# Kernel tuning notes

Hardware: AMD Instinct MI355X
Metric: run time of the kernel (lower is better)

Reference implementation:

```python
import jax, jax.numpy as jnp
import numpy as np

BLOCK = 64      # block_size
NRAND = 3       # num_random_blocks
NUM_HEAD = 16
HEAD_DIM = 64
HIDDEN = 1024
PEN = -10000.0  # HF attn_mask_penalty


def _sparse_attn(q, k, v, band_mask, from_mask, to_mask, blocked_mask, rand_attn):
    # q,k,v: [B,H,S,D]; BigBird block-sparse attention (HF math).
    B, H, S, D = q.shape
    b, r = BLOCK, NRAND
    n = S // b
    rsd = 1.0 / (D ** 0.5)

    bq = q.reshape(B, H, n, b, D)
    bk = k.reshape(B, H, n, b, D)
    bv = v.reshape(B, H, n, b, D)

    bi = jnp.arange(B)[:, None, None, None]
    hi = jnp.arange(H)[None, :, None, None]
    # gathered random key/value blocks: [B,H,n-2,r*b,D]
    gk = bk[bi, hi, rand_attn].reshape(B, H, n - 2, r * b, D)
    gv = bv[bi, hi, rand_attn].reshape(B, H, n - 2, r * b, D)
    # random-block mask: [B,H,n-2,b,r*b]
    rm = blocked_mask[bi, rand_attn].reshape(B, H, n - 2, r * b)
    rand_mask = jnp.einsum("blq,bhlk->bhlqk", blocked_mask[:, 1:-1], rm)

    ones = lambda shp: jnp.ones(shp, q.dtype)

    # ---- first query block: attends to everything ----
    p = jnp.einsum("bhqd,bhkd->bhqk", bq[:, :, 0], k) * rsd + (1.0 - to_mask) * PEN
    c0 = jnp.einsum("bhqk,bhkd->bhqd", jax.nn.softmax(p, -1), v)[:, :, None]

    # ---- second query block: blocks 0,1,2,last + random ----
    k1 = jnp.concatenate([bk[:, :, 0], bk[:, :, 1], bk[:, :, 2], bk[:, :, -1], gk[:, :, 0]], axis=2)
    v1 = jnp.concatenate([bv[:, :, 0], bv[:, :, 1], bv[:, :, 2], bv[:, :, -1], gv[:, :, 0]], axis=2)
    p = jnp.einsum("bhqd,bhkd->bhqk", bq[:, :, 1], k1) * rsd
    seq_pad = jnp.concatenate([to_mask[..., :3 * b], to_mask[..., -b:], ones((B, 1, 1, r * b))], axis=3)
    rand_pad = jnp.concatenate([ones((B, H, b, 4 * b)), rand_mask[:, :, 0]], axis=3)
    p = p + (1.0 - jnp.minimum(seq_pad, rand_pad)) * PEN
    c1 = jnp.einsum("bhqk,bhkd->bhqd", jax.nn.softmax(p, -1), v1)[:, :, None]

    # ---- middle blocks 2..n-3: band(3 blocks) + first + last + random ----
    ek = jnp.concatenate([bk[:, :, 1:-3], bk[:, :, 2:-2], bk[:, :, 3:-1]], axis=3)  # [B,H,n-4,3b,D]
    ev = jnp.concatenate([bv[:, :, 1:-3], bv[:, :, 2:-2], bv[:, :, 3:-1]], axis=3)
    mq = bq[:, :, 2:-2]                                                              # [B,H,n-4,b,D]
    inner = jnp.einsum("bhlqd,bhlkd->bhlqk", mq, ek) * rsd + (1.0 - band_mask) * PEN
    randp = jnp.einsum("bhlqd,bhlkd->bhlqk", mq, gk[:, :, 1:-1]) * rsd + (1.0 - rand_mask[:, :, 1:-1]) * PEN
    firstp = jnp.einsum("bhlqd,bhkd->bhlqk", mq, bk[:, :, 0]) * rsd + (1.0 - to_mask[..., :b][:, :, None]) * PEN
    lastp = jnp.einsum("bhlqd,bhkd->bhlqk", mq, bk[:, :, -1]) * rsd + (1.0 - to_mask[..., -b:][:, :, None]) * PEN
    band = jnp.concatenate([firstp, inner, randp, lastp], axis=-1)  # [B,H,n-4,b,(5+r)*b]
    a = jax.nn.softmax(band, -1)
    cm = jnp.einsum("bhlqk,bhlkd->bhlqd", a[..., b:4 * b], ev)
    cm = cm + jnp.einsum("bhlqk,bhlkd->bhlqd", a[..., 4 * b:-b], gv[:, :, 1:-1])
    cm = cm + jnp.einsum("bhlqk,bhkd->bhlqd", a[..., :b], bv[:, :, 0])
    cm = cm + jnp.einsum("bhlqk,bhkd->bhlqd", a[..., -b:], bv[:, :, -1])

    # ---- second-last query block: blocks 0,-3,-2,-1 + random ----
    k2 = jnp.concatenate([bk[:, :, 0], bk[:, :, -3], bk[:, :, -2], bk[:, :, -1], gk[:, :, -1]], axis=2)
    v2 = jnp.concatenate([bv[:, :, 0], bv[:, :, -3], bv[:, :, -2], bv[:, :, -1], gv[:, :, -1]], axis=2)
    p = jnp.einsum("bhqd,bhkd->bhqk", bq[:, :, -2], k2) * rsd
    seq_pad = jnp.concatenate([to_mask[..., :b], to_mask[..., -3 * b:], ones((B, 1, 1, r * b))], axis=3)
    rand_pad = jnp.concatenate([ones((B, H, b, 4 * b)), rand_mask[:, :, -1]], axis=3)
    p = p + (1.0 - jnp.minimum(seq_pad, rand_pad)) * PEN
    c2 = jnp.einsum("bhqk,bhkd->bhqd", jax.nn.softmax(p, -1), v2)[:, :, None]

    # ---- last query block: attends to everything ----
    p = jnp.einsum("bhqd,bhkd->bhqk", bq[:, :, -1], k) * rsd + (1.0 - to_mask) * PEN
    c3 = jnp.einsum("bhqk,bhkd->bhqd", jax.nn.softmax(p, -1), v)[:, :, None]

    ctx = jnp.concatenate([c0, c1, cm, c2, c3], axis=2).reshape(B, H, S, D)
    ctx = ctx * from_mask  # [B,1,S,1]
    return ctx.transpose(0, 2, 1, 3).reshape(B, S, H * D)


def setup_inputs() -> dict:
    key = jax.random.key(0)
    ks = jax.random.split(key, 12)
    B, L = 2, 4064
    S = 4096
    n = S // BLOCK
    sc = 0.02
    inp = {
        "X": jax.random.normal(ks[0], (B, L, HIDDEN), jnp.float32),
        "Wq": jax.random.normal(ks[1], (HIDDEN, NUM_HEAD * HEAD_DIM), jnp.float32) * sc,
        "b_q": jnp.zeros((NUM_HEAD * HEAD_DIM,), jnp.float32),
        "Wk": jax.random.normal(ks[2], (HIDDEN, NUM_HEAD * HEAD_DIM), jnp.float32) * sc,
        "b_k": jnp.zeros((NUM_HEAD * HEAD_DIM,), jnp.float32),
        "Wv": jax.random.normal(ks[3], (HIDDEN, NUM_HEAD * HEAD_DIM), jnp.float32) * sc,
        "b_v": jnp.zeros((NUM_HEAD * HEAD_DIM,), jnp.float32),
        "Wo": jax.random.normal(ks[4], (NUM_HEAD * HEAD_DIM, HIDDEN), jnp.float32) * sc,
        "b_o": jnp.zeros((HIDDEN,), jnp.float32),
        "band_mask": jnp.ones((B, 1, n - 4, BLOCK, 3 * BLOCK), jnp.float32),
        "from_mask": jnp.ones((B, 1, S, 1), jnp.float32),
        "to_mask": jnp.ones((B, 1, 1, S), jnp.float32),
        "blocked_encoder_mask": jnp.ones((B, n, BLOCK), jnp.float32),
        "rand_attn": jax.random.randint(ks[5], (B, NUM_HEAD, n - 2, NRAND), 0, n, jnp.int32),
    }
    return inp


def reference(X, Wq, b_q, Wk, b_k, Wv, b_v, Wo, b_o,
              band_mask, from_mask, to_mask, blocked_encoder_mask, rand_attn):
    B, L, _ = X.shape
    pad = BLOCK - L % BLOCK  # matches torch wrapper (pads full block if L % b == 0)
    Xp = jnp.pad(X, ((0, 0), (0, pad), (0, 0)))
    S = L + pad

    def proj(W, bias):
        return (Xp @ W + bias).reshape(B, S, NUM_HEAD, HEAD_DIM).transpose(0, 2, 1, 3)

    q, k, v = proj(Wq, b_q), proj(Wk, b_k), proj(Wv, b_v)
    attn = _sparse_attn(q, k, v, band_mask, from_mask, to_mask, blocked_encoder_mask, rand_attn)
    out = attn @ Wo + b_o
    return out[:, :L]
```

## Files before the change

### kernel.cpp

```cpp
#include <hip/hip_runtime.h>

#define BB 2
#define SEQ 4096
#define LQ 4064
#define HID 1024
#define NH 16
#define HD 64
#define NB 64
#define BLK 64
#define NR 3
#define PENV -10000.0f

typedef __bf16 bf16;
typedef __bf16 bf16x8 __attribute__((ext_vector_type(8)));
typedef float floatx4 __attribute__((ext_vector_type(4)));

__device__ inline floatx4 mfma16(bf16x8 a, bf16x8 b, floatx4 c) {
    return __builtin_amdgcn_mfma_f32_16x16x32_bf16(a, b, c, 0, 0, 0);
}

__device__ inline void async_ld16(const bf16* g, bf16* l) {
    __builtin_amdgcn_global_load_lds(
        (const __attribute__((address_space(1))) unsigned int*)g,
        (__attribute__((address_space(3))) unsigned int*)l, 16, 0, 0);
}

__global__ __launch_bounds__(256) void cast_pad_x(const float* __restrict__ X,
                                                  bf16* __restrict__ Xp) {
    int t = blockIdx.x * 256 + threadIdx.x;
    int c4 = t & 255;
    int row = t >> 8;
    int b = row >> 12;
    int s = row & 4095;
    float4 v = make_float4(0.f, 0.f, 0.f, 0.f);
    if (s < LQ) {
        v = reinterpret_cast<const float4*>(X + ((size_t)(b * LQ + s)) * HID)[c4];
    }
    union { bf16 h[4]; uint2 u; } o;
    o.h[0] = (bf16)v.x; o.h[1] = (bf16)v.y; o.h[2] = (bf16)v.z; o.h[3] = (bf16)v.w;
    *reinterpret_cast<uint2*>(Xp + (size_t)row * HID + c4 * 4) = o.u;
}

__global__ __launch_bounds__(256) void transpose_w(const float* __restrict__ Wq,
                                                   const float* __restrict__ Wk,
                                                   const float* __restrict__ Wv,
                                                   const float* __restrict__ Wo,
                                                   bf16* __restrict__ WqkvT,
                                                   bf16* __restrict__ WoT) {
    __shared__ float tile[64][65];
    int sel = blockIdx.z;
    const float* src = (sel == 0) ? Wq : (sel == 1) ? Wk : (sel == 2) ? Wv : Wo;
    bf16* dst = (sel < 3) ? (WqkvT + (size_t)sel * HID * HID) : WoT;
    int j0 = blockIdx.x * 64, k0 = blockIdx.y * 64;
    int tx = threadIdx.x, ty = threadIdx.y;
    for (int i = 0; i < 16; i++) {
        int k = ty + i * 4;
        tile[k][tx] = src[(size_t)(k0 + k) * HID + j0 + tx];
    }
    __syncthreads();
    for (int i = 0; i < 16; i++) {
        int j = ty + i * 4;
        dst[(size_t)(j0 + j) * HID + k0 + tx] = (bf16)tile[tx][j];
    }
}

__global__ __launch_bounds__(256) void transpose_band(const float* __restrict__ band,
                                                      float* __restrict__ bandT) {
    __shared__ float tile[64][65];
    int kt = blockIdx.x;
    int lrow = blockIdx.y;
    int b = blockIdx.z;
    const float* src = band + ((size_t)(b * (NB - 4) + lrow) * BLK) * 192;
    float* dst = bandT + ((size_t)(b * (NB - 4) + lrow) * 192) * BLK;
    int tx = threadIdx.x, ty = threadIdx.y;
    for (int i = 0; i < 16; i++) {
        int qq = i * 4 + ty;
        tile[qq][tx] = src[(size_t)qq * 192 + kt * 64 + tx];
    }
    __syncthreads();
    for (int i = 0; i < 16; i++) {
        int k = i * 4 + ty;
        dst[(size_t)(kt * 64 + k) * BLK + tx] = tile[tx][k];
    }
}

__global__ __launch_bounds__(256) void gemm_qkv(const bf16* __restrict__ Xp,
                                                const bf16* __restrict__ WT,
                                                const float* __restrict__ bq,
                                                const float* __restrict__ bk,
                                                const float* __restrict__ bv,
                                                bf16* __restrict__ qo,
                                                bf16* __restrict__ ko,
                                                bf16* __restrict__ vt) {
    __shared__ __align__(16) char smem[36864];
    bf16* As = (bf16*)smem;
    bf16* Bs = As + 128 * 64;
    int tid = threadIdx.x;
    int wave = tid >> 6, lane = tid & 63;
    int quad = lane >> 4, lm = lane & 15;
    int id = blockIdx.x;
    int xcd = id & 7, slot = id >> 3;
    int tile_m = (xcd * 8 + (slot & 7)) * 128;
    int tile_n = (slot >> 3) * 128;
    int wm = (wave & 1) * 64, wn = (wave >> 1) * 64;

    floatx4 acc[4][4] = {};

    for (int k0 = 0; k0 < HID; k0 += 64) {
        __syncthreads();
        for (int it = 0; it < 4; it++) {
            int c = it * 256 + tid;
            int row = c >> 3, col = (c & 7) * 8;
            async_ld16(Xp + (size_t)(tile_m + row) * HID + k0 + col, &As[c * 8]);
            async_ld16(WT + (size_t)(tile_n + row) * HID + k0 + col, &Bs[c * 8]);
        }
        __syncthreads();
        for (int ks = 0; ks < 64; ks += 32) {
            bf16x8 a[4], b[4];
            for (int i = 0; i < 4; i++)
                a[i] = *reinterpret_cast<const bf16x8*>(&As[(wm + i * 16 + lm) * 64 + ks + quad * 8]);
            for (int j = 0; j < 4; j++)
                b[j] = *reinterpret_cast<const bf16x8*>(&Bs[(wn + j * 16 + lm) * 64 + ks + quad * 8]);
            for (int i = 0; i < 4; i++)
                for (int j = 0; j < 4; j++)
                    acc[i][j] = mfma16(a[i], b[j], acc[i][j]);
        }
    }

    int which = tile_n >> 10;
    int hc_base = (tile_n + wn) & 1023;
    int h = hc_base >> 6;
    const float* bias = (which == 0) ? bq : (which == 1) ? bk : bv;
    __syncthreads();
    bf16* ep = (bf16*)smem + wave * (64 * 72);

    if (which < 2) {
        #pragma unroll
        for (int i = 0; i < 4; i++)
            #pragma unroll
            for (int j = 0; j < 4; j++) {
                float bsv = bias[hc_base + j * 16 + lm];
                #pragma unroll
                for (int r = 0; r < 4; r++) {
                    float val = acc[i][j][r] + bsv;
                    if (which == 0) val *= 0.125f;
                    ep[(i * 16 + quad * 4 + r) * 72 + j * 16 + lm] = (bf16)val;
                }
            }
        __builtin_amdgcn_wave_barrier();
        int s_glob = tile_m + wm + lane;
        int b_ = s_glob >> 12, s = s_glob & 4095;
        bf16* dstb = ((which == 0) ? qo : ko) + ((size_t)((b_ * NH + h) * SEQ + s)) * HD;
        #pragma unroll
        for (int c = 0; c < 8; c++)
            *reinterpret_cast<uint4*>(dstb + c * 8) =
                *reinterpret_cast<const uint4*>(ep + lane * 72 + c * 8);
    } else {
        #pragma unroll
        for (int i = 0; i < 4; i++)
            #pragma unroll
            for (int j = 0; j < 4; j++) {
                float bsv = bias[hc_base + j * 16 + lm];
                #pragma unroll
                for (int r = 0; r < 4; r++) {
                    float val = acc[i][j][r] + bsv;
                    ep[(j * 16 + lm) * 72 + i * 16 + quad * 4 + r] = (bf16)val;
                }
            }
        __builtin_amdgcn_wave_barrier();
        int s_base = tile_m + wm;
        int b_ = s_base >> 12, s0 = s_base & 4095;
        bf16* dstb = vt + ((size_t)((b_ * NH + h) * HD + lane)) * SEQ + s0;
        #pragma unroll
        for (int c = 0; c < 8; c++)
            *reinterpret_cast<uint4*>(dstb + c * 8) =
                *reinterpret_cast<const uint4*>(ep + lane * 72 + c * 8);
    }
}

__global__ __launch_bounds__(256, 2) void attn_kernel(const bf16* __restrict__ q,
                                                      const bf16* __restrict__ kk,
                                                      const bf16* __restrict__ vt,
                                                      const float* __restrict__ bandT,
                                                      const float* __restrict__ fromm,
                                                      const float* __restrict__ tom,
                                                      const float* __restrict__ blocked,
                                                      const int* __restrict__ rand_attn,
                                                      bf16* __restrict__ attn) {
    __shared__ __align__(16) char smem[33792 + 512];

    int tid = threadIdx.x, wave = tid >> 6, lane = tid & 63;
    int quad = lane >> 4, lm = lane & 15;
    int bh = blockIdx.x;
    int b = bh >> 4, h = bh & 15;
    size_t bh_base = (size_t)bh * SEQ * HD;
    int x = blockIdx.y;
    bool fullmode = (x < 8);
    int l, sub;
    if (fullmode) { l = (x >> 2) ? (NB - 1) : 0; sub = x & 3; }
    else          { l = x - 7;                   sub = wave;  }

    bf16x8 aq0 = *reinterpret_cast<const bf16x8*>(
        q + bh_base + (size_t)(l * BLK + sub * 16 + lm) * HD + quad * 8);
    bf16x8 aq1 = *reinterpret_cast<const bf16x8*>(
        q + bh_base + (size_t)(l * BLK + sub * 16 + lm) * HD + 32 + quad * 8);

    floatx4 ctx[4] = {};
    float mrun = -1e30f, lrun = 0.f;
    float mq = blocked[((size_t)b * NB + l) * BLK + sub * 16 + lm];

    int blist[8], btype[8];
    if (!fullmode) {
        int base;
        if (l == 1) {
            blist[0] = 0; blist[1] = 1; blist[2] = 2; blist[3] = NB - 1;
            btype[0] = btype[1] = btype[2] = btype[3] = 0;
            base = 4;
        } else if (l == NB - 2) {
            blist[0] = 0; blist[1] = NB - 3; blist[2] = NB - 2; blist[3] = NB - 1;
            btype[0] = btype[1] = btype[2] = btype[3] = 0;
            base = 4;
        } else {
            blist[0] = 0;      btype[0] = 0;
            blist[1] = l - 1;  btype[1] = 1;
            blist[2] = l;      btype[2] = 2;
            blist[3] = l + 1;  btype[3] = 3;
            blist[4] = NB - 1; btype[4] = 0;
            base = 5;
        }
        const int* ra = rand_attn + ((size_t)(b * NH + h) * (NB - 2) + (l - 1)) * NR;
        for (int r = 0; r < NR; r++) { blist[base + r] = ra[r]; btype[base + r] = 4; }
        for (int i = base + NR; i < 8; i++) { blist[i] = 0; btype[i] = 5; }
    }

    bf16* pw = (bf16*)smem + wave * 16 * 264;

    int nch = fullmode ? 4 : 2;
    for (int ch = 0; ch < nch; ch++) {
        floatx4 sc[4][4];
        #pragma unroll
        for (int ib = 0; ib < 4; ib++) {
            int kb  = fullmode ? (wave * 16 + ch * 4 + ib) : blist[ch * 4 + ib];
            int typ = fullmode ? 0 : btype[ch * 4 + ib];
            const bf16* kbase = kk + bh_base + (size_t)kb * BLK * HD;
            #pragma unroll
            for (int f = 0; f < 4; f++) {
                bf16x8 a0 = *reinterpret_cast<const bf16x8*>(kbase + (f * 16 + lm) * HD + quad * 8);
                bf16x8 a1 = *reinterpret_cast<const bf16x8*>(kbase + (f * 16 + lm) * HD + 32 + quad * 8);
                floatx4 z = {0.f, 0.f, 0.f, 0.f};
                z = mfma16(a0, aq0, z);
                z = mfma16(a1, aq1, z);
                sc[ib][f] = z;
            }
            if (typ == 0) {
                #pragma unroll
                for (int f = 0; f < 4; f++) {
                    float4 t4 = *reinterpret_cast<const float4*>(
                        tom + (size_t)b * SEQ + kb * BLK + f * 16 + quad * 4);
                    sc[ib][f][0] += (1.f - t4.x) * PENV;
                    sc[ib][f][1] += (1.f - t4.y) * PENV;
                    sc[ib][f][2] += (1.f - t4.z) * PENV;
                    sc[ib][f][3] += (1.f - t4.w) * PENV;
                }
            } else if (typ == 4) {
                #pragma unroll
                for (int f = 0; f < 4; f++) {
                    float4 t4 = *reinterpret_cast<const float4*>(
                        blocked + ((size_t)b * NB + kb) * BLK + f * 16 + quad * 4);
                    sc[ib][f][0] += (1.f - mq * t4.x) * PENV;
                    sc[ib][f][1] += (1.f - mq * t4.y) * PENV;
                    sc[ib][f][2] += (1.f - mq * t4.z) * PENV;
                    sc[ib][f][3] += (1.f - mq * t4.w) * PENV;
                }
            } else if (typ != 5) {
                int t = typ - 1;
                const float* bp = bandT + ((size_t)(b * (NB - 4) + (l - 2)) * 192 + t * 64) * BLK;
                #pragma unroll
                for (int f = 0; f < 4; f++)
                    #pragma unroll
                    for (int r = 0; r < 4; r++) {
                        float bm = bp[(size_t)(f * 16 + quad * 4 + r) * BLK + sub * 16 + lm];
                        sc[ib][f][r] += (1.f - bm) * PENV;
                    }
            } else {
                #pragma unroll
                for (int f = 0; f < 4; f++)
                    #pragma unroll
                    for (int r = 0; r < 4; r++) sc[ib][f][r] += PENV;
            }
        }

        float mx = -1e30f;
        #pragma unroll
        for (int ib = 0; ib < 4; ib++)
            #pragma unroll
            for (int f = 0; f < 4; f++)
                #pragma unroll
                for (int r = 0; r < 4; r++) mx = fmaxf(mx, sc[ib][f][r]);
        mx = fmaxf(mx, __shfl_xor(mx, 16, 64));
        mx = fmaxf(mx, __shfl_xor(mx, 32, 64));
        float mnew = fmaxf(mrun, mx);
        float scale = __expf(mrun - mnew);
        lrun *= scale;
        #pragma unroll
        for (int dj = 0; dj < 4; dj++) ctx[dj] *= scale;
        mrun = mnew;

        __builtin_amdgcn_wave_barrier();
        float rs = 0.f;
        #pragma unroll
        for (int ib = 0; ib < 4; ib++)
            #pragma unroll
            for (int f = 0; f < 4; f++) {
                float p0 = __expf(sc[ib][f][0] - mnew);
                float p1 = __expf(sc[ib][f][1] - mnew);
                float p2 = __expf(sc[ib][f][2] - mnew);
                float p3 = __expf(sc[ib][f][3] - mnew);
                rs += (p0 + p1) + (p2 + p3);
                union { bf16 hh[4]; uint2 u; } pu;
                pu.hh[0] = (bf16)p0; pu.hh[1] = (bf16)p1;
                pu.hh[2] = (bf16)p2; pu.hh[3] = (bf16)p3;
                *reinterpret_cast<uint2*>(pw + lm * 264 + ib * 64 + f * 16 + quad * 4) = pu.u;
            }
        __builtin_amdgcn_wave_barrier();
        rs += __shfl_xor(rs, 16, 64);
        rs += __shfl_xor(rs, 32, 64);
        lrun += rs;

        #pragma unroll
        for (int ib = 0; ib < 4; ib++) {
            int kb = fullmode ? (wave * 16 + ch * 4 + ib) : blist[ch * 4 + ib];
            const bf16* vtb = vt + (size_t)bh * HD * SEQ + (size_t)kb * BLK;
            bf16x8 pb0 = *reinterpret_cast<const bf16x8*>(pw + lm * 264 + ib * 64 + quad * 8);
            bf16x8 pb1 = *reinterpret_cast<const bf16x8*>(pw + lm * 264 + ib * 64 + 32 + quad * 8);
            #pragma unroll
            for (int dj = 0; dj < 4; dj++) {
                bf16x8 aV0 = *reinterpret_cast<const bf16x8*>(
                    vtb + (size_t)(dj * 16 + lm) * SEQ + quad * 8);
                bf16x8 aV1 = *reinterpret_cast<const bf16x8*>(
                    vtb + (size_t)(dj * 16 + lm) * SEQ + 32 + quad * 8);
                ctx[dj] = mfma16(aV0, pb0, ctx[dj]);
                ctx[dj] = mfma16(aV1, pb1, ctx[dj]);
            }
        }
    }

    if (!fullmode) {
        int sq = l * BLK + sub * 16 + lm;
        float w = (1.f / lrun) * fromm[(size_t)b * SEQ + sq];
        bf16* dst = attn + ((size_t)(b * SEQ + sq)) * HID + h * HD;
        #pragma unroll
        for (int dj = 0; dj < 4; dj++) {
            union { bf16 hh[4]; uint2 u; } o;
            #pragma unroll
            for (int r = 0; r < 4; r++) o.hh[r] = (bf16)(ctx[dj][r] * w);
            *reinterpret_cast<uint2*>(dst + dj * 16 + quad * 4) = o.u;
        }
    } else {
        float* ctxL = (float*)smem;
        float* mL   = (float*)(smem + 33792);
        float* lL   = (float*)(smem + 33792 + 256);
        __syncthreads();
        #pragma unroll
        for (int dj = 0; dj < 4; dj++)
            #pragma unroll
            for (int r = 0; r < 4; r++)
                ctxL[wave * 1024 + (dj * 16 + quad * 4 + r) * 16 + lm] = ctx[dj][r];
        if (quad == 0) { mL[wave * 16 + lm] = mrun; lL[wave * 16 + lm] = lrun; }
        __syncthreads();
        int qq = tid & 15, dbase = (tid >> 4) * 4;
        float M = -1e30f;
        for (int w = 0; w < 4; w++) M = fmaxf(M, mL[w * 16 + qq]);
        float e[4], Lt = 0.f;
        for (int w = 0; w < 4; w++) { e[w] = __expf(mL[w * 16 + qq] - M); Lt += lL[w * 16 + qq] * e[w]; }
        int sq = l * BLK + sub * 16 + qq;
        float wgt = (1.f / Lt) * fromm[(size_t)b * SEQ + sq];
        union { bf16 hh[4]; uint2 u; } o;
        #pragma unroll
        for (int dd = 0; dd < 4; dd++) {
            float acc = 0.f;
            for (int w = 0; w < 4; w++) acc += ctxL[w * 1024 + (dbase + dd) * 16 + qq] * e[w];
            o.hh[dd] = (bf16)(acc * wgt);
        }
        *reinterpret_cast<uint2*>(attn + ((size_t)(b * SEQ + sq)) * HID + h * HD + dbase) = o.u;
    }
}

__global__ __launch_bounds__(256) void gemm_out(const bf16* __restrict__ A,
                                                const bf16* __restrict__ WoT,
                                                const float* __restrict__ bo,
                                                float* __restrict__ out) {
    __shared__ __align__(16) bf16 As[128 * 64];
    __shared__ __align__(16) bf16 Bs[128 * 64];
    int tid = threadIdx.x;
    int wave = tid >> 6, lane = tid & 63;
    int quad = lane >> 4, lm = lane & 15;
    int id = blockIdx.x;
    int xcd = id & 7, slot = id >> 3;
    int tile_m = (xcd * 8 + (slot & 7)) * 128;
    int tile_n = (slot >> 3) * 128;
    int wm = (wave & 1) * 64, wn = (wave >> 1) * 64;

    floatx4 acc[4][4] = {};

    for (int k0 = 0; k0 < HID; k0 += 64) {
        __syncthreads();
        for (int it = 0; it < 4; it++) {
            int c = it * 256 + tid;
            int row = c >> 3, col = (c & 7) * 8;
            async_ld16(A + (size_t)(tile_m + row) * HID + k0 + col, &As[c * 8]);
            async_ld16(WoT + (size_t)(tile_n + row) * HID + k0 + col, &Bs[c * 8]);
        }
        __syncthreads();
        for (int ks = 0; ks < 64; ks += 32) {
            bf16x8 a[4], b[4];
            for (int i = 0; i < 4; i++)
                a[i] = *reinterpret_cast<const bf16x8*>(&As[(wm + i * 16 + lm) * 64 + ks + quad * 8]);
            for (int j = 0; j < 4; j++)
                b[j] = *reinterpret_cast<const bf16x8*>(&Bs[(wn + j * 16 + lm) * 64 + ks + quad * 8]);
            for (int i = 0; i < 4; i++)
                for (int j = 0; j < 4; j++)
                    acc[i][j] = mfma16(a[i], b[j], acc[i][j]);
        }
    }

    for (int i = 0; i < 4; i++) {
        for (int j = 0; j < 4; j++) {
            int nn = tile_n + wn + j * 16 + lm;
            float bsv = bo[nn];
            for (int r = 0; r < 4; r++) {
                int mm = tile_m + wm + i * 16 + quad * 4 + r;
                int b_ = mm >> 12, s = mm & 4095;
                if (s < LQ)
                    out[((size_t)(b_ * LQ + s)) * HID + nn] = acc[i][j][r] + bsv;
            }
        }
    }
}

extern "C" void kernel_launch(void* const* d_in, const int* in_sizes, int n_in,
                              void* d_out, int out_size, void* d_ws, size_t ws_size,
                              hipStream_t stream) {
    const float* X       = (const float*)d_in[0];
    const float* Wq      = (const float*)d_in[1];
    const float* bq      = (const float*)d_in[2];
    const float* Wk      = (const float*)d_in[3];
    const float* bk      = (const float*)d_in[4];
    const float* Wv      = (const float*)d_in[5];
    const float* bv      = (const float*)d_in[6];
    const float* Wo      = (const float*)d_in[7];
    const float* bo      = (const float*)d_in[8];
    const float* band    = (const float*)d_in[9];
    const float* fromm   = (const float*)d_in[10];
    const float* tom     = (const float*)d_in[11];
    const float* blocked = (const float*)d_in[12];
    const int*   randa   = (const int*)d_in[13];
    float* out = (float*)d_out;

    char* ws = (char*)d_ws;
    bf16* Xp    = (bf16*)(ws + 0);
    bf16* WqkvT = (bf16*)(ws + 16777216);
    bf16* WoT   = (bf16*)(ws + 23068672);
    bf16* qb    = (bf16*)(ws + 25165824);
    bf16* kb    = (bf16*)(ws + 41943040);
    bf16* vtb   = (bf16*)(ws + 58720256);
    bf16* attnb = Xp;
    float* bandT = (float*)WqkvT;

    cast_pad_x<<<dim3(8192), dim3(256), 0, stream>>>(X, Xp);
    transpose_w<<<dim3(16, 16, 4), dim3(64, 4), 0, stream>>>(Wq, Wk, Wv, Wo, WqkvT, WoT);
    gemm_qkv<<<dim3(1536), dim3(256), 0, stream>>>(Xp, WqkvT, bq, bk, bv, qb, kb, vtb);
    transpose_band<<<dim3(3, NB - 4, BB), dim3(64, 4), 0, stream>>>(band, bandT);
    attn_kernel<<<dim3(BB * NH, 70), dim3(256), 0, stream>>>(qb, kb, vtb, bandT, fromm, tom,
                                                             blocked, randa, attnb);
    gemm_out<<<dim3(512), dim3(256), 0, stream>>>(attnb, WoT, bo, out);
}
```

Before: 398.2 us.

## Split attention key blocks across 8 waves and skip all-ones masks

Doubles the attention workgroup from 4 to 8 waves. Each query sub-block's key blocks are split between two waves, which halves the serial chunk loop per wave, and the partial softmax states are merged in shared memory at the end. Also adds a small kernel that checks whether the to/blocked/band masks are all ones and sets per-batch flags. When a flag is set, the attention kernel skips loading and applying that mask. The mask skipping is still checked at runtime, so results stay correct, but it adds an extra launch and a full read of the band mask.

```diff
diff --git a/kernel.cpp b/kernel.cpp
--- a/kernel.cpp
+++ b/kernel.cpp
@@ -82,6 +82,32 @@
         int k = i * 4 + ty;
         dst[(size_t)(kt * 64 + k) * BLK + tx] = tile[tx][k];
     }
+}
+
+__global__ __launch_bounds__(256) void mask_flags(const float* __restrict__ tom,
+                                                  const float* __restrict__ blocked,
+                                                  const float* __restrict__ band,
+                                                  int* __restrict__ flags) {
+    int which = blockIdx.x, b = blockIdx.y;
+    const float* src;
+    size_t n;
+    if (which == 0)      { src = tom     + (size_t)b * SEQ;                  n = SEQ; }
+    else if (which == 1) { src = blocked + (size_t)b * NB * BLK;             n = NB * BLK; }
+    else                 { src = band    + (size_t)b * (NB - 4) * BLK * 192; n = (size_t)(NB - 4) * BLK * 192; }
+    const float4* s4 = (const float4*)src;
+    size_t n4 = n >> 2;
+    int ok = 1;
+    for (size_t i = threadIdx.x; i < n4; i += 256) {
+        float4 v = s4[i];
+        ok &= (v.x == 1.0f) & (v.y == 1.0f) & (v.z == 1.0f) & (v.w == 1.0f);
+    }
+    ok = __all(ok) ? 1 : 0;
+    __shared__ int sh;
+    if (threadIdx.x == 0) sh = 1;
+    __syncthreads();
+    if ((threadIdx.x & 63) == 0 && !ok) atomicAnd(&sh, 0);
+    __syncthreads();
+    if (threadIdx.x == 0) flags[which * BB + b] = sh;
 }
 
 __global__ __launch_bounds__(256) void gemm_qkv(const bf16* __restrict__ Xp,
@@ -178,7 +204,7 @@
     }
 }
 
-__global__ __launch_bounds__(256, 2) void attn_kernel(const bf16* __restrict__ q,
+__global__ __launch_bounds__(512, 4) void attn_kernel(const bf16* __restrict__ q,
                                                       const bf16* __restrict__ kk,
                                                       const bf16* __restrict__ vt,
                                                       const float* __restrict__ bandT,
@@ -186,19 +212,24 @@
                                                       const float* __restrict__ tom,
                                                       const float* __restrict__ blocked,
                                                       const int* __restrict__ rand_attn,
+                                                      const int* __restrict__ flags,
                                                       bf16* __restrict__ attn) {
-    __shared__ __align__(16) char smem[33792 + 512];
+    __shared__ __align__(16) char smem[34816 + 1024];
 
     int tid = threadIdx.x, wave = tid >> 6, lane = tid & 63;
     int quad = lane >> 4, lm = lane & 15;
     int bh = blockIdx.x;
     int b = bh >> 4, h = bh & 15;
     size_t bh_base = (size_t)bh * SEQ * HD;
-    int x = blockIdx.y;
-    bool fullmode = (x < 8);
-    int l, sub;
-    if (fullmode) { l = (x >> 2) ? (NB - 1) : 0; sub = x & 3; }
-    else          { l = x - 7;                   sub = wave;  }
+    int y = blockIdx.y;
+    bool fullmode = (y < 8);
+    int l, sub, half;
+    if (fullmode) { l = (y >> 2) ? (NB - 1) : 0; sub = y & 3;    half = 0; }
+    else          { l = y - 7;                   sub = wave & 3; half = wave >> 2; }
+
+    bool sk_to = flags[b] != 0;
+    bool sk_bl = flags[2 + b] != 0;
+    bool sk_bd = flags[4 + b] != 0;
 
     bf16x8 aq0 = *reinterpret_cast<const bf16x8*>(
         q + bh_base + (size_t)(l * BLK + sub * 16 + lm) * HD + quad * 8);
@@ -233,15 +264,15 @@
         for (int i = base + NR; i < 8; i++) { blist[i] = 0; btype[i] = 5; }
     }
 
-    bf16* pw = (bf16*)smem + wave * 16 * 264;
-
-    int nch = fullmode ? 4 : 2;
+    bf16* pw = (bf16*)smem + wave * 16 * 136;
+
+    int nch = fullmode ? 2 : 1;
     for (int ch = 0; ch < nch; ch++) {
         floatx4 sc[4][4];
         #pragma unroll
         for (int ib = 0; ib < 4; ib++) {
-            int kb  = fullmode ? (wave * 16 + ch * 4 + ib) : blist[ch * 4 + ib];
-            int typ = fullmode ? 0 : btype[ch * 4 + ib];
+            int kb  = fullmode ? (wave * 8 + ch * 4 + ib) : blist[half * 4 + ib];
+            int typ = fullmode ? 0 : btype[half * 4 + ib];
             const bf16* kbase = kk + bh_base + (size_t)kb * BLK * HD;
             #pragma unroll
             for (int f = 0; f < 4; f++) {
@@ -253,35 +284,41 @@
                 sc[ib][f] = z;
             }
             if (typ == 0) {
-                #pragma unroll
-                for (int f = 0; f < 4; f++) {
-                    float4 t4 = *reinterpret_cast<const float4*>(
-                        tom + (size_t)b * SEQ + kb * BLK + f * 16 + quad * 4);
-                    sc[ib][f][0] += (1.f - t4.x) * PENV;
-                    sc[ib][f][1] += (1.f - t4.y) * PENV;
-                    sc[ib][f][2] += (1.f - t4.z) * PENV;
-                    sc[ib][f][3] += (1.f - t4.w) * PENV;
+                if (!sk_to) {
+                    #pragma unroll
+                    for (int f = 0; f < 4; f++) {
+                        float4 t4 = *reinterpret_cast<const float4*>(
+                            tom + (size_t)b * SEQ + kb * BLK + f * 16 + quad * 4);
+                        sc[ib][f][0] += (1.f - t4.x) * PENV;
+                        sc[ib][f][1] += (1.f - t4.y) * PENV;
+                        sc[ib][f][2] += (1.f - t4.z) * PENV;
+                        sc[ib][f][3] += (1.f - t4.w) * PENV;
+                    }
                 }
             } else if (typ == 4) {
-                #pragma unroll
-                for (int f = 0; f < 4; f++) {
-                    float4 t4 = *reinterpret_cast<const float4*>(
-                        blocked + ((size_t)b * NB + kb) * BLK + f * 16 + quad * 4);
-                    sc[ib][f][0] += (1.f - mq * t4.x) * PENV;
-                    sc[ib][f][1] += (1.f - mq * t4.y) * PENV;
-                    sc[ib][f][2] += (1.f - mq * t4.z) * PENV;
-                    sc[ib][f][3] += (1.f - mq * t4.w) * PENV;
+                if (!sk_bl) {
+                    #pragma unroll
+                    for (int f = 0; f < 4; f++) {
+                        float4 t4 = *reinterpret_cast<const float4*>(
+                            blocked + ((size_t)b * NB + kb) * BLK + f * 16 + quad * 4);
+                        sc[ib][f][0] += (1.f - mq * t4.x) * PENV;
+                        sc[ib][f][1] += (1.f - mq * t4.y) * PENV;
+                        sc[ib][f][2] += (1.f - mq * t4.z) * PENV;
+                        sc[ib][f][3] += (1.f - mq * t4.w) * PENV;
+                    }
                 }
             } else if (typ != 5) {
-                int t = typ - 1;
-                const float* bp = bandT + ((size_t)(b * (NB - 4) + (l - 2)) * 192 + t * 64) * BLK;
-                #pragma unroll
-                for (int f = 0; f < 4; f++)
+                if (!sk_bd) {
+                    int t = typ - 1;
+                    const float* bp = bandT + ((size_t)(b * (NB - 4) + (l - 2)) * 192 + t * 64) * BLK;
                     #pragma unroll
-                    for (int r = 0; r < 4; r++) {
-                        float bm = bp[(size_t)(f * 16 + quad * 4 + r) * BLK + sub * 16 + lm];
-                        sc[ib][f][r] += (1.f - bm) * PENV;
-                    }
+                    for (int f = 0; f < 4; f++)
+                        #pragma unroll
+                        for (int r = 0; r < 4; r++) {
+                            float bm = bp[(size_t)(f * 16 + quad * 4 + r) * BLK + sub * 16 + lm];
+                            sc[ib][f][r] += (1.f - bm) * PENV;
+                        }
+                }
             } else {
                 #pragma unroll
                 for (int f = 0; f < 4; f++)
@@ -306,83 +343,95 @@
         for (int dj = 0; dj < 4; dj++) ctx[dj] *= scale;
         mrun = mnew;
 
-        __builtin_amdgcn_wave_barrier();
         float rs = 0.f;
         #pragma unroll
-        for (int ib = 0; ib < 4; ib++)
+        for (int p = 0; p < 2; p++) {
+            __builtin_amdgcn_wave_barrier();
             #pragma unroll
-            for (int f = 0; f < 4; f++) {
-                float p0 = __expf(sc[ib][f][0] - mnew);
-                float p1 = __expf(sc[ib][f][1] - mnew);
-                float p2 = __expf(sc[ib][f][2] - mnew);
-                float p3 = __expf(sc[ib][f][3] - mnew);
-                rs += (p0 + p1) + (p2 + p3);
-                union { bf16 hh[4]; uint2 u; } pu;
-                pu.hh[0] = (bf16)p0; pu.hh[1] = (bf16)p1;
-                pu.hh[2] = (bf16)p2; pu.hh[3] = (bf16)p3;
-                *reinterpret_cast<uint2*>(pw + lm * 264 + ib * 64 + f * 16 + quad * 4) = pu.u;
-            }
-        __builtin_amdgcn_wave_barrier();
+            for (int k2 = 0; k2 < 2; k2++) {
+                int ib = p * 2 + k2;
+                #pragma unroll
+                for (int f = 0; f < 4; f++) {
+                    float p0 = __expf(sc[ib][f][0] - mnew);
+                    float p1 = __expf(sc[ib][f][1] - mnew);
+                    float p2 = __expf(sc[ib][f][2] - mnew);
+                    float p3 = __expf(sc[ib][f][3] - mnew);
+                    rs += (p0 + p1) + (p2 + p3);
+                    union { bf16 hh[4]; uint2 u; } pu;
+                    pu.hh[0] = (bf16)p0; pu.hh[1] = (bf16)p1;
+                    pu.hh[2] = (bf16)p2; pu.hh[3] = (bf16)p3;
+                    *reinterpret_cast<uint2*>(pw + lm * 136 + k2 * 64 + f * 16 + quad * 4) = pu.u;
+                }
+            }
+            __builtin_amdgcn_wave_barrier();
+            #pragma unroll
+            for (int k2 = 0; k2 < 2; k2++) {
+                int ib = p * 2 + k2;
+                int kb = fullmode ? (wave * 8 + ch * 4 + ib) : blist[half * 4 + ib];
+                const bf16* vtb = vt + (size_t)bh * HD * SEQ + (size_t)kb * BLK;
+                bf16x8 pb0 = *reinterpret_cast<const bf16x8*>(pw + lm * 136 + k2 * 64 + quad * 8);
+                bf16x8 pb1 = *reinterpret_cast<const bf16x8*>(pw + lm * 136 + k2 * 64 + 32 + quad * 8);
+                #pragma unroll
+                for (int dj = 0; dj < 4; dj++) {
+                    bf16x8 aV0 = *reinterpret_cast<const bf16x8*>(
+                        vtb + (size_t)(dj * 16 + lm) * SEQ + quad * 8);
+                    bf16x8 aV1 = *reinterpret_cast<const bf16x8*>(
+                        vtb + (size_t)(dj * 16 + lm) * SEQ + 32 + quad * 8);
+                    ctx[dj] = mfma16(aV0, pb0, ctx[dj]);
+                    ctx[dj] = mfma16(aV1, pb1, ctx[dj]);
+                }
+            }
+        }
         rs += __shfl_xor(rs, 16, 64);
         rs += __shfl_xor(rs, 32, 64);
         lrun += rs;
-
-        #pragma unroll
-        for (int ib = 0; ib < 4; ib++) {
-            int kb = fullmode ? (wave * 16 + ch * 4 + ib) : blist[ch * 4 + ib];
-            const bf16* vtb = vt + (size_t)bh * HD * SEQ + (size_t)kb * BLK;
-            bf16x8 pb0 = *reinterpret_cast<const bf16x8*>(pw + lm * 264 + ib * 64 + quad * 8);
-            bf16x8 pb1 = *reinterpret_cast<const bf16x8*>(pw + lm * 264 + ib * 64 + 32 + quad * 8);
-            #pragma unroll
-            for (int dj = 0; dj < 4; dj++) {
-                bf16x8 aV0 = *reinterpret_cast<const bf16x8*>(
-                    vtb + (size_t)(dj * 16 + lm) * SEQ + quad * 8);
-                bf16x8 aV1 = *reinterpret_cast<const bf16x8*>(
-                    vtb + (size_t)(dj * 16 + lm) * SEQ + 32 + quad * 8);
-                ctx[dj] = mfma16(aV0, pb0, ctx[dj]);
-                ctx[dj] = mfma16(aV1, pb1, ctx[dj]);
-            }
-        }
-    }
-
-    if (!fullmode) {
-        int sq = l * BLK + sub * 16 + lm;
-        float w = (1.f / lrun) * fromm[(size_t)b * SEQ + sq];
-        bf16* dst = attn + ((size_t)(b * SEQ + sq)) * HID + h * HD;
-        #pragma unroll
-        for (int dj = 0; dj < 4; dj++) {
-            union { bf16 hh[4]; uint2 u; } o;
-            #pragma unroll
-            for (int r = 0; r < 4; r++) o.hh[r] = (bf16)(ctx[dj][r] * w);
-            *reinterpret_cast<uint2*>(dst + dj * 16 + quad * 4) = o.u;
-        }
-    } else {
-        float* ctxL = (float*)smem;
-        float* mL   = (float*)(smem + 33792);
-        float* lL   = (float*)(smem + 33792 + 256);
-        __syncthreads();
-        #pragma unroll
-        for (int dj = 0; dj < 4; dj++)
-            #pragma unroll
-            for (int r = 0; r < 4; r++)
-                ctxL[wave * 1024 + (dj * 16 + quad * 4 + r) * 16 + lm] = ctx[dj][r];
-        if (quad == 0) { mL[wave * 16 + lm] = mrun; lL[wave * 16 + lm] = lrun; }
-        __syncthreads();
-        int qq = tid & 15, dbase = (tid >> 4) * 4;
+    }
+
+    float* ctxL = (float*)smem;
+    float* mL   = (float*)(smem + 32768);
+    float* lL   = (float*)(smem + 32768 + 512);
+    __syncthreads();
+    #pragma unroll
+    for (int dj = 0; dj < 4; dj++)
+        #pragma unroll
+        for (int r = 0; r < 4; r++)
+            ctxL[wave * 1024 + (dj * 16 + quad * 4 + r) * 16 + lm] = ctx[dj][r];
+    if (quad == 0) { mL[wave * 16 + lm] = mrun; lL[wave * 16 + lm] = lrun; }
+    __syncthreads();
+
+    if (fullmode) {
+        int qq = tid & 15, dbase = (tid >> 4) * 2;
         float M = -1e30f;
-        for (int w = 0; w < 4; w++) M = fmaxf(M, mL[w * 16 + qq]);
-        float e[4], Lt = 0.f;
-        for (int w = 0; w < 4; w++) { e[w] = __expf(mL[w * 16 + qq] - M); Lt += lL[w * 16 + qq] * e[w]; }
+        for (int w = 0; w < 8; w++) M = fmaxf(M, mL[w * 16 + qq]);
+        float e[8], Lt = 0.f;
+        for (int w = 0; w < 8; w++) { e[w] = __expf(mL[w * 16 + qq] - M); Lt += lL[w * 16 + qq] * e[w]; }
         int sq = l * BLK + sub * 16 + qq;
         float wgt = (1.f / Lt) * fromm[(size_t)b * SEQ + sq];
-        union { bf16 hh[4]; uint2 u; } o;
-        #pragma unroll
-        for (int dd = 0; dd < 4; dd++) {
+        union { bf16 hh[2]; unsigned int u; } o;
+        #pragma unroll
+        for (int dd = 0; dd < 2; dd++) {
             float acc = 0.f;
-            for (int w = 0; w < 4; w++) acc += ctxL[w * 1024 + (dbase + dd) * 16 + qq] * e[w];
+            for (int w = 0; w < 8; w++) acc += ctxL[w * 1024 + (dbase + dd) * 16 + qq] * e[w];
             o.hh[dd] = (bf16)(acc * wgt);
         }
-        *reinterpret_cast<uint2*>(attn + ((size_t)(b * SEQ + sq)) * HID + h * HD + dbase) = o.u;
+        *reinterpret_cast<unsigned int*>(attn + ((size_t)(b * SEQ + sq)) * HID + h * HD + dbase) = o.u;
+    } else {
+        int s = tid >> 7, t = tid & 127;
+        int qq = t & 15, dbase = (t >> 4) * 8;
+        float m0 = mL[s * 16 + qq], m1 = mL[(s + 4) * 16 + qq];
+        float M = fmaxf(m0, m1);
+        float e0 = __expf(m0 - M), e1 = __expf(m1 - M);
+        float Lt = lL[s * 16 + qq] * e0 + lL[(s + 4) * 16 + qq] * e1;
+        int sq = l * BLK + s * 16 + qq;
+        float wgt = (1.f / Lt) * fromm[(size_t)b * SEQ + sq];
+        union { bf16 hh[8]; uint4 u; } o;
+        #pragma unroll
+        for (int dd = 0; dd < 8; dd++) {
+            float acc = ctxL[s * 1024 + (dbase + dd) * 16 + qq] * e0
+                      + ctxL[(s + 4) * 1024 + (dbase + dd) * 16 + qq] * e1;
+            o.hh[dd] = (bf16)(acc * wgt);
+        }
+        *reinterpret_cast<uint4*>(attn + ((size_t)(b * SEQ + sq)) * HID + h * HD + dbase) = o.u;
     }
 }
 
@@ -466,12 +515,14 @@
     bf16* vtb   = (bf16*)(ws + 58720256);
     bf16* attnb = Xp;
     float* bandT = (float*)WqkvT;
+    int* flagsp = (int*)(ws + 16777216 + 5898240);
 
     cast_pad_x<<<dim3(8192), dim3(256), 0, stream>>>(X, Xp);
     transpose_w<<<dim3(16, 16, 4), dim3(64, 4), 0, stream>>>(Wq, Wk, Wv, Wo, WqkvT, WoT);
     gemm_qkv<<<dim3(1536), dim3(256), 0, stream>>>(Xp, WqkvT, bq, bk, bv, qb, kb, vtb);
     transpose_band<<<dim3(3, NB - 4, BB), dim3(64, 4), 0, stream>>>(band, bandT);
-    attn_kernel<<<dim3(BB * NH, 70), dim3(256), 0, stream>>>(qb, kb, vtb, bandT, fromm, tom,
-                                                             blocked, randa, attnb);
+    mask_flags<<<dim3(3, BB), dim3(256), 0, stream>>>(tom, blocked, band, flagsp);
+    attn_kernel<<<dim3(BB * NH, 70), dim3(512), 0, stream>>>(qb, kb, vtb, bandT, fromm, tom,
+                                                             blocked, randa, flagsp, attnb);
     gemm_out<<<dim3(512), dim3(256), 0, stream>>>(attnb, WoT, bo, out);
 }
```

Result: slower. 646.6 us (+62.4%).
